# Optimization experiments

Measured on AMD Instinct MI355X. Metric: run time of the kernel, lower is better.

The kernel has to match this reference:

```python
import jax, jax.numpy as jnp
import numpy as np

N_CLASSES = 2  # FS-MOL binary labels


def setup_inputs() -> dict:
    key = jax.random.key(0)
    k1, k2, k3 = jax.random.split(key, 3)
    Ns, Nq, d = 512, 16384, 512
    support_features = jax.random.normal(k1, (Ns, d), dtype=jnp.float32)
    support_labels = jax.random.randint(k2, (Ns,), 0, N_CLASSES, dtype=jnp.int64)
    query_features = jax.random.normal(k3, (Nq, d), dtype=jnp.float32)
    return {
        "support_features": support_features,
        "support_labels": support_labels,
        "query_features": query_features,
    }


def _cov(x):
    # rowvar=False covariance of [N, d] -> [d, d], matching _estimate_cov
    xc = x - jnp.mean(x, axis=0, keepdims=True)
    return (xc.T @ xc) / (x.shape[0] - 1)


def reference(support_features, support_labels, query_features):
    d = support_features.shape[1]
    dt = support_features.dtype
    task_cov = _cov(support_features)          # [d, d]
    reg = jnp.asarray(0.1, dt) * jnp.eye(d, dtype=dt)

    def per_class(c):
        mask = (support_labels == c).astype(dt)            # [Ns]
        n = mask.sum()                                      # scalar count
        mean = (mask[:, None] * support_features).sum(0) / n
        xc = (support_features - mean) * mask[:, None]      # zero out other classes
        cov_c = (xc.T @ xc) / (n - 1.0)
        lam = jnp.minimum(n / (n + 1.0), jnp.asarray(0.1, dt))
        prec = jnp.linalg.inv(lam * cov_c + (1.0 - lam) * task_cov + reg)
        return mean, prec

    means, precs = jax.vmap(per_class)(jnp.arange(N_CLASSES))  # [C,d], [C,d,d]

    # Mahalanobis: diff[c,q,:] = mean_c - query_q  (matches repeated_class_means - repeated_target)
    diff = means[:, None, :] - query_features[None, :, :]      # [C, Nq, d]
    h = jnp.einsum('cqd,cde->cqe', diff, precs)                # [C, Nq, d]
    logits = -(h * diff).sum(-1).T                             # [Nq, C]
    return logits
```

## Files before the change

kernel.cpp:

```cpp
#include <hip/hip_runtime.h>

#define NS 512
#define DF 512
#define NQ 16384

#define WS_MEAN0 0
#define WS_MEAN1 512
#define WS_MEANA 1024
#define WS_CNT   1536
#define WS_V0    2048
#define WS_V1    2560
#define WS_KC    3072
#define WS_M     4096
#define WS_PB    (WS_M + 2*DF*DF)
#define WS_QB    (WS_PB + DF*DF)
#define WS_GP    WS_QB
#define WS_SCR   WS_QB

typedef __attribute__((ext_vector_type(8))) short short8;
typedef __attribute__((ext_vector_type(4))) float floatx4;

__device__ __forceinline__ unsigned short f2bf(float f) {
    unsigned u = __float_as_uint(f);
    unsigned r = (u + 0x7fffu + ((u >> 16) & 1u)) >> 16;
    return (unsigned short)r;
}

__device__ __forceinline__ float readlane_f(float v, int lane) {
    return __uint_as_float(__builtin_amdgcn_readlane(__float_as_uint(v), lane));
}

__device__ __forceinline__ void load_lds16(const void* g, void* l) {
    __builtin_amdgcn_global_load_lds(
        (const __attribute__((address_space(1))) unsigned int*)g,
        (__attribute__((address_space(3))) unsigned int*)l, 16, 0, 0);
}

__device__ __forceinline__ void gj_invert64(float* T, float (*rbuf)[4][64], int tid) {
    int jl = tid & 63, w = tid >> 6;
    float Tr[16];
    if (w < 4) {
#pragma unroll
        for (int m = 0; m < 16; ++m) Tr[m] = T[(w * 16 + m) * 66 + jl];
    }
#pragma unroll
    for (int r = 0; r < 16; ++r) {
        const int q0 = r * 4;
        const int par = r & 1;
        if (w == (q0 >> 4)) {
            const int mb = q0 & 15;
            rbuf[par][0][jl] = Tr[mb + 0];
            rbuf[par][1][jl] = Tr[mb + 1];
            rbuf[par][2][jl] = Tr[mb + 2];
            rbuf[par][3][jl] = Tr[mb + 3];
        }
        __syncthreads();
        if (w < 4) {
            float B[4][4];
#pragma unroll
            for (int a = 0; a < 4; ++a)
#pragma unroll
                for (int bb = 0; bb < 4; ++bb) B[a][bb] = rbuf[par][a][q0 + bb];
#pragma unroll
            for (int p = 0; p < 4; ++p) {
                float piv = 1.0f / B[p][p];
#pragma unroll
                for (int j = 0; j < 4; ++j) if (j != p) B[p][j] *= piv;
#pragma unroll
                for (int i = 0; i < 4; ++i) if (i != p) {
                    float f = B[i][p];
#pragma unroll
                    for (int j = 0; j < 4; ++j) if (j != p) B[i][j] -= f * B[p][j];
                    B[i][p] = -f * piv;
                }
                B[p][p] = piv;
            }
            float r0v = rbuf[par][0][jl], r1v = rbuf[par][1][jl];
            float r2v = rbuf[par][2][jl], r3v = rbuf[par][3][jl];
            float nr[4];
#pragma unroll
            for (int a = 0; a < 4; ++a)
                nr[a] = B[a][0] * r0v + B[a][1] * r1v + B[a][2] * r2v + B[a][3] * r3v;
            bool colin = ((jl >> 2) == r);
            int bsel = jl & 3;
            float Bc[4];
#pragma unroll
            for (int a = 0; a < 4; ++a)
                Bc[a] = bsel == 0 ? B[a][0]
                      : (bsel == 1 ? B[a][1] : (bsel == 2 ? B[a][2] : B[a][3]));
#pragma unroll
            for (int m = 0; m < 16; ++m) {
                float cv0 = readlane_f(Tr[m], q0 + 0);
                float cv1 = readlane_f(Tr[m], q0 + 1);
                float cv2 = readlane_f(Tr[m], q0 + 2);
                float cv3 = readlane_f(Tr[m], q0 + 3);
                float g = Tr[m] - (cv0 * nr[0] + cv1 * nr[1] + cv2 * nr[2] + cv3 * nr[3]);
                bool rowin = (((w * 16 + m) >> 2) == r);
                float gcol = -(cv0 * Bc[0] + cv1 * Bc[1] + cv2 * Bc[2] + cv3 * Bc[3]);
                if (rowin) g = nr[m & 3];
                if (colin) g = rowin ? Bc[m & 3] : gcol;
                Tr[m] = g;
            }
        }
    }
    if (w < 4) {
#pragma unroll
        for (int m = 0; m < 16; ++m) T[(w * 16 + m) * 66 + jl] = Tr[m];
    }
    __syncthreads();
}

__global__ __launch_bounds__(256) void k_front(const float* __restrict__ S,
                                               const int* __restrict__ lab,
                                               float* __restrict__ ws) {
    int b = blockIdx.x, tid = threadIdx.x;
    if (b >= 512) {
        __shared__ int slb[NS];
        __shared__ float r0[4][64], r1[4][64];
        __shared__ int rc[4];
        int bs = b - 512;
        for (int l = tid; l < NS; l += 256) slb[l] = lab[l];
        __syncthreads();
        int dl = tid & 63, ch = tid >> 6;
        int dd = bs * 64 + dl;
        float s0 = 0.f, s1 = 0.f;
        int n1 = 0;
        for (int n = ch * 128; n < ch * 128 + 128; ++n) {
            float v = S[n * DF + dd];
            if (slb[n]) { s1 += v; n1++; } else { s0 += v; }
        }
        r0[ch][dl] = s0; r1[ch][dl] = s1;
        if (dl == 0) rc[ch] = n1;
        __syncthreads();
        if (ch == 0) {
            float t0 = 0.f, t1 = 0.f; int n1t = 0;
#pragma unroll
            for (int x = 0; x < 4; ++x) { t0 += r0[x][dl]; t1 += r1[x][dl]; n1t += rc[x]; }
            float fn1 = (float)n1t, fn0 = (float)(NS - n1t);
            ws[WS_MEAN0 + dd] = t0 / fn0;
            ws[WS_MEAN1 + dd] = t1 / fn1;
            ws[WS_MEANA + dd] = (t0 + t1) / (float)NS;
            if (bs == 0 && dl == 0) {
                ws[WS_CNT] = fn0; ws[WS_CNT + 1] = fn1;
                ws[WS_KC] = 0.f; ws[WS_KC + 1] = 0.f;
            }
        }
        return;
    }
    __shared__ float SA[16 * 65];
    __shared__ float SB[16 * 65];
    __shared__ int lb[16];
    int tx = tid & 15, ty = tid >> 4;
    int i0 = (b & 7) * 64, j0 = ((b >> 3) & 7) * 64;
    int z = b >> 6;
    float a0[4][4] = {{0.f}}, a1[4][4] = {{0.f}};
    for (int nc = z * 64; nc < z * 64 + 64; nc += 16) {
#pragma unroll
        for (int l = 0; l < 4; ++l) {
            int idx = tid + 256 * l;
            int nn = idx >> 6, col = idx & 63;
            SA[nn * 65 + col] = S[(nc + nn) * DF + i0 + col];
            SB[nn * 65 + col] = S[(nc + nn) * DF + j0 + col];
        }
        if (tid < 16) lb[tid] = lab[nc + tid];
        __syncthreads();
#pragma unroll
        for (int kk = 0; kk < 16; ++kk) {
            float av[4], bv[4];
#pragma unroll
            for (int r = 0; r < 4; ++r) av[r] = SA[kk * 65 + ty * 4 + r];
#pragma unroll
            for (int s = 0; s < 4; ++s) bv[s] = SB[kk * 65 + tx * 4 + s];
            if (lb[kk]) {
#pragma unroll
                for (int r = 0; r < 4; ++r)
#pragma unroll
                    for (int s = 0; s < 4; ++s) a1[r][s] += av[r] * bv[s];
            } else {
#pragma unroll
                for (int r = 0; r < 4; ++r)
#pragma unroll
                    for (int s = 0; s < 4; ++s) a0[r][s] += av[r] * bv[s];
            }
        }
        __syncthreads();
    }
    float* Gp = ws + WS_GP;
#pragma unroll
    for (int r = 0; r < 4; ++r) {
        int i = i0 + ty * 4 + r;
#pragma unroll
        for (int s = 0; s < 4; ++s) {
            int j = j0 + tx * 4 + s;
            Gp[((z * 2 + 0) * DF + i) * DF + j] = a0[r][s];
            Gp[((z * 2 + 1) * DF + i) * DF + j] = a1[r][s];
        }
    }
}

__global__ __launch_bounds__(256) void k_asm(float* __restrict__ ws) {
    const float* Gp = ws + WS_GP;
    int e = blockIdx.x * 256 + threadIdx.x;
    int i = e >> 9, j = e & 511;
    float g0 = 0.f, g1 = 0.f;
#pragma unroll
    for (int ch = 0; ch < 8; ++ch) {
        g0 += Gp[((ch * 2 + 0) * DF + i) * DF + j];
        g1 += Gp[((ch * 2 + 1) * DF + i) * DF + j];
    }
    float n0 = ws[WS_CNT], n1 = ws[WS_CNT + 1];
    float lam0 = fminf(n0 / (n0 + 1.f), 0.1f);
    float lam1 = fminf(n1 / (n1 + 1.f), 0.1f);
    float m0i = ws[WS_MEAN0 + i], m1i = ws[WS_MEAN1 + i], mai = ws[WS_MEANA + i];
    float m0j = ws[WS_MEAN0 + j], m1j = ws[WS_MEAN1 + j], maj = ws[WS_MEANA + j];
    float task = (g0 + g1 - (float)NS * mai * maj) / (float)(NS - 1);
    float cov0 = (g0 - n0 * m0i * m0j) / (n0 - 1.f);
    float cov1 = (g1 - n1 * m1i * m1j) / (n1 - 1.f);
    float dg = (i == j) ? 0.1f : 0.f;
    ws[WS_M + i * DF + j] = lam0 * cov0 + (1.f - lam0) * task + dg;
    ws[WS_M + DF * DF + i * DF + j] = lam1 * cov1 + (1.f - lam1) * task + dg;
}

__global__ __launch_bounds__(256) void k_pivot0(float* __restrict__ ws) {
    int c = blockIdx.x;
    __shared__ float T[64 * 66];
    __shared__ float rbuf[2][4][64];
    const float* Akk = ws + WS_M + (size_t)c * DF * DF;
    int tid = threadIdx.x;
#pragma unroll
    for (int m = 0; m < 16; ++m) {
        int idx = tid + 256 * m;
        int i = idx >> 6, j = idx & 63;
        T[i * 66 + j] = Akk[i * DF + j];
    }
    __syncthreads();
    gj_invert64(T, rbuf, tid);
    float* scr = ws + WS_SCR + (0 * 2 + c) * 4096;
#pragma unroll
    for (int m = 0; m < 16; ++m) {
        int idx = tid + 256 * m;
        int i = idx >> 6, j = idx & 63;
        scr[i * 64 + j] = T[i * 66 + j];
    }
}

__global__ __launch_bounds__(512) void k_updA(float* __restrict__ ws, int k, int wbf) {
    int c = blockIdx.y, jh = blockIdx.z;
    int ti = blockIdx.x >> 3, tj = blockIdx.x & 7;
    if (ti == k || tj == k) return;
    float* Mb = ws + WS_M + (size_t)c * DF * DF;
    unsigned short* pb = (unsigned short*)(ws + WS_PB) + (size_t)c * DF * DF;
    const float* scr_in = ws + WS_SCR + ((k & 1) * 2 + c) * 4096;
    int tid = threadIdx.x;
    __shared__ float T[64 * 66];
    __shared__ float LV[64 * 65];
    __shared__ float LU[64 * 34];
    __shared__ float D1[64 * 34];
#pragma unroll
    for (int m = 0; m < 8; ++m) {
        int idx = tid + 512 * m;
        int i = idx >> 6, j = idx & 63;
        T[i * 66 + j] = scr_in[i * 64 + j];
    }
    {
        const float* src = Mb + (ti * 64) * DF + k * 64;
#pragma unroll
        for (int m = 0; m < 8; ++m) {
            int idx = tid + 512 * m;
            int i = idx >> 6, j = idx & 63;
            LV[i * 65 + j] = src[i * DF + j];
        }
    }
    {
        const float* src = Mb + (k * 64) * DF + tj * 64 + jh * 32;
#pragma unroll
        for (int m = 0; m < 4; ++m) {
            int idx = tid + 512 * m;
            int i = idx >> 5, j = idx & 31;
            LU[i * 34 + j] = src[i * DF + j];
        }
    }
    __syncthreads();
    int tx16 = tid & 15, ty32 = tid >> 4;
    int cb0 = jh * 32;
    float a1[2][2] = {{0.f}};
#pragma unroll 8
    for (int kk = 0; kk < 64; ++kk) {
        float av0 = T[(ty32 * 2 + 0) * 66 + kk];
        float av1 = T[(ty32 * 2 + 1) * 66 + kk];
        float2 bv = *(const float2*)&LU[kk * 34 + tx16 * 2];
        a1[0][0] += av0 * bv.x; a1[0][1] += av0 * bv.y;
        a1[1][0] += av1 * bv.x; a1[1][1] += av1 * bv.y;
    }
#pragma unroll
    for (int r = 0; r < 2; ++r)
        *(float2*)&D1[(ty32 * 2 + r) * 34 + tx16 * 2] = make_float2(a1[r][0], a1[r][1]);
    __syncthreads();
    float a2[2][2] = {{0.f}};
#pragma unroll 8
    for (int kk = 0; kk < 64; ++kk) {
        float av0 = LV[(ty32 * 2 + 0) * 65 + kk];
        float av1 = LV[(ty32 * 2 + 1) * 65 + kk];
        float2 bv = *(const float2*)&D1[kk * 34 + tx16 * 2];
        a2[0][0] += av0 * bv.x; a2[0][1] += av0 * bv.y;
        a2[1][0] += av1 * bv.x; a2[1][1] += av1 * bv.y;
    }
    float* dst = Mb + (ti * 64) * DF + tj * 64 + cb0;
#pragma unroll
    for (int r = 0; r < 2; ++r) {
        float2 old = *(const float2*)&dst[(ty32 * 2 + r) * DF + tx16 * 2];
        float nv0 = old.x - a2[r][0], nv1 = old.y - a2[r][1];
        *(float2*)&dst[(ty32 * 2 + r) * DF + tx16 * 2] = make_float2(nv0, nv1);
        if (wbf) {
            unsigned up = (unsigned)f2bf(nv0) | ((unsigned)f2bf(nv1) << 16);
            *(unsigned*)&pb[(size_t)(ti * 64 + ty32 * 2 + r) * DF + tj * 64 + cb0 + tx16 * 2] = up;
        }
    }
}

__global__ __launch_bounds__(512) void k_updB(float* __restrict__ ws, int k, int wbf) {
    int c = blockIdx.y, jh = blockIdx.z;
    int x = blockIdx.x;
    int tid = threadIdx.x;
    __shared__ float T[64 * 66];
    __shared__ float X[64 * 65];
    float* Mb = ws + WS_M + (size_t)c * DF * DF;
    unsigned short* pb = (unsigned short*)(ws + WS_PB) + (size_t)c * DF * DF;
    const float* scr_in = ws + WS_SCR + ((k & 1) * 2 + c) * 4096;

    if (x == 16) {
        if (jh == 1 || k == 7) return;
        const float* src = Mb + ((k + 1) * 64) * DF + (k + 1) * 64;
#pragma unroll
        for (int m = 0; m < 8; ++m) {
            int idx = tid + 512 * m;
            int i = idx >> 6, j = idx & 63;
            T[i * 66 + j] = src[i * DF + j];
        }
        __syncthreads();
        gj_invert64(T, (float(*)[4][64])X, tid);
        float* scr_out = ws + WS_SCR + (((k + 1) & 1) * 2 + c) * 4096;
#pragma unroll
        for (int m = 0; m < 8; ++m) {
            int idx = tid + 512 * m;
            int i = idx >> 6, j = idx & 63;
            scr_out[i * 64 + j] = T[i * 66 + j];
        }
        return;
    }
    int cb0 = jh * 32;
    int tx16 = tid & 15, ty32 = tid >> 4;
    if (x < 8) {
        int tj = x;
        if (tj == k) {
            float* Akk = Mb + (k * 64) * DF + k * 64;
#pragma unroll
            for (int m = 0; m < 4; ++m) {
                int idx = tid + 512 * m;
                int i = idx >> 5, j = idx & 31;
                float v = scr_in[i * 64 + cb0 + j];
                Akk[i * DF + cb0 + j] = v;
                if (wbf) pb[(size_t)(k * 64 + i) * DF + k * 64 + cb0 + j] = f2bf(v);
            }
            return;
        }
#pragma unroll
        for (int m = 0; m < 8; ++m) {
            int idx = tid + 512 * m;
            int i = idx >> 6, j = idx & 63;
            T[i * 66 + j] = scr_in[i * 64 + j];
        }
        {
            const float* src = Mb + (k * 64) * DF + tj * 64 + cb0;
#pragma unroll
            for (int m = 0; m < 4; ++m) {
                int idx = tid + 512 * m;
                int i = idx >> 5, j = idx & 31;
                X[i * 34 + j] = src[i * DF + j];
            }
        }
        __syncthreads();
        float acc[2][2] = {{0.f}};
#pragma unroll 8
        for (int kk = 0; kk < 64; ++kk) {
            float av0 = T[(ty32 * 2 + 0) * 66 + kk];
            float av1 = T[(ty32 * 2 + 1) * 66 + kk];
            float2 bv = *(const float2*)&X[kk * 34 + tx16 * 2];
            acc[0][0] += av0 * bv.x; acc[0][1] += av0 * bv.y;
            acc[1][0] += av1 * bv.x; acc[1][1] += av1 * bv.y;
        }
        float* dst = Mb + (k * 64) * DF + tj * 64 + cb0;
#pragma unroll
        for (int r = 0; r < 2; ++r) {
            *(float2*)&dst[(ty32 * 2 + r) * DF + tx16 * 2] = make_float2(acc[r][0], acc[r][1]);
            if (wbf) {
                unsigned up = (unsigned)f2bf(acc[r][0]) | ((unsigned)f2bf(acc[r][1]) << 16);
                *(unsigned*)&pb[(size_t)(k * 64 + ty32 * 2 + r) * DF + tj * 64 + cb0 + tx16 * 2] = up;
            }
        }
    } else {
        int ti = x - 8;
        if (ti == k || jh == 1) return;
#pragma unroll
        for (int m = 0; m < 8; ++m) {
            int idx = tid + 512 * m;
            int i = idx >> 6, j = idx & 63;
            T[i * 66 + j] = scr_in[i * 64 + j];
        }
        {
            const float* src = Mb + (ti * 64) * DF + k * 64;
#pragma unroll
            for (int m = 0; m < 8; ++m) {
                int idx = tid + 512 * m;
                int i = idx >> 6, j = idx & 63;
                X[i * 65 + j] = src[i * DF + j];
            }
        }
        __syncthreads();
        float acc[2][2][2];
#pragma unroll
        for (int p = 0; p < 2; ++p)
#pragma unroll
            for (int r = 0; r < 2; ++r) { acc[p][r][0] = 0.f; acc[p][r][1] = 0.f; }
#pragma unroll 4
        for (int kk = 0; kk < 64; ++kk) {
            float av0 = X[(ty32 * 2 + 0) * 65 + kk];
            float av1 = X[(ty32 * 2 + 1) * 65 + kk];
            float2 b0 = *(const float2*)&T[kk * 66 + tx16 * 2];
            float2 b1 = *(const float2*)&T[kk * 66 + 32 + tx16 * 2];
            acc[0][0][0] += av0 * b0.x; acc[0][0][1] += av0 * b0.y;
            acc[0][1][0] += av1 * b0.x; acc[0][1][1] += av1 * b0.y;
            acc[1][0][0] += av0 * b1.x; acc[1][0][1] += av0 * b1.y;
            acc[1][1][0] += av1 * b1.x; acc[1][1][1] += av1 * b1.y;
        }
        float* dst = Mb + (ti * 64) * DF + k * 64;
#pragma unroll
        for (int p = 0; p < 2; ++p)
#pragma unroll
            for (int r = 0; r < 2; ++r) {
                int row = ty32 * 2 + r, col = p * 32 + tx16 * 2;
                float v0 = -acc[p][r][0], v1 = -acc[p][r][1];
                *(float2*)&dst[row * DF + col] = make_float2(v0, v1);
                if (wbf) {
                    unsigned up = (unsigned)f2bf(v0) | ((unsigned)f2bf(v1) << 16);
                    *(unsigned*)&pb[(size_t)(ti * 64 + row) * DF + k * 64 + col] = up;
                }
            }
    }
}

__global__ __launch_bounds__(256) void k_vk(float* __restrict__ ws) {
    int c = blockIdx.x >> 3, rb = blockIdx.x & 7;
    const float* P = ws + WS_M + (size_t)c * DF * DF;
    const float* mc = ws + (c ? WS_MEAN1 : WS_MEAN0);
    float* v = ws + (c ? WS_V1 : WS_V0);
    __shared__ float ml[DF];
    __shared__ float red[4][64];
    int tid = threadIdx.x;
    for (int l = tid; l < DF; l += 256) ml[l] = mc[l];
    __syncthreads();
    int rl = tid & 63, ch = tid >> 6;
    int row = rb * 64 + rl;
    float dot = 0.f;
    const float* pr = P + (size_t)row * DF + ch * 128;
    for (int t = 0; t < 32; ++t) {
        float4 pv = *(const float4*)(pr + t * 4);
        const float* mm = ml + ch * 128 + t * 4;
        dot += pv.x * mm[0] + pv.y * mm[1] + pv.z * mm[2] + pv.w * mm[3];
    }
    red[ch][rl] = dot;
    __syncthreads();
    if (ch == 0) {
        float d = red[0][rl] + red[1][rl] + red[2][rl] + red[3][rl];
        v[row] = d;
        float kp = d * ml[row];
#pragma unroll
        for (int off = 32; off > 0; off >>= 1) kp += __shfl_down(kp, off);
        if (rl == 0) atomicAdd(&ws[WS_KC + c], kp);
    }
}

__global__ __launch_bounds__(256) void k_qinit(const float* __restrict__ Q,
                                               float* __restrict__ ws,
                                               float* __restrict__ out) {
    unsigned short* qbw = (unsigned short*)(ws + WS_QB);
    const float* v0 = ws + WS_V0;
    const float* v1 = ws + WS_V1;
    int lane = threadIdx.x & 63;
    int q = blockIdx.x * 4 + (threadIdx.x >> 6);
    const float* qrow = Q + (size_t)q * DF + lane * 8;
    float4 x0 = *(const float4*)(qrow);
    float4 x1 = *(const float4*)(qrow + 4);
    const float* v0p = v0 + lane * 8;
    const float* v1p = v1 + lane * 8;
    float4 w00 = *(const float4*)(v0p), w01 = *(const float4*)(v0p + 4);
    float4 w10 = *(const float4*)(v1p), w11 = *(const float4*)(v1p + 4);
    float a0 = x0.x * w00.x + x0.y * w00.y + x0.z * w00.z + x0.w * w00.w
             + x1.x * w01.x + x1.y * w01.y + x1.z * w01.z + x1.w * w01.w;
    float a1 = x0.x * w10.x + x0.y * w10.y + x0.z * w10.z + x0.w * w10.w
             + x1.x * w11.x + x1.y * w11.y + x1.z * w11.z + x1.w * w11.w;
    short8 r;
    r[0] = (short)f2bf(x0.x); r[1] = (short)f2bf(x0.y);
    r[2] = (short)f2bf(x0.z); r[3] = (short)f2bf(x0.w);
    r[4] = (short)f2bf(x1.x); r[5] = (short)f2bf(x1.y);
    r[6] = (short)f2bf(x1.z); r[7] = (short)f2bf(x1.w);
    *(short8*)(qbw + (size_t)q * DF + lane * 8) = r;
#pragma unroll
    for (int off = 32; off > 0; off >>= 1) {
        a0 += __shfl_down(a0, off);
        a1 += __shfl_down(a1, off);
    }
    if (lane == 0) {
        out[q * 2 + 0] = 2.f * a0 - ws[WS_KC + 0];
        out[q * 2 + 1] = 2.f * a1 - ws[WS_KC + 1];
    }
}

__global__ __launch_bounds__(256, 3) void k_gemm(const float* __restrict__ ws,
                                                 float* __restrict__ out) {
    const unsigned short* qb = (const unsigned short*)(ws + WS_QB);
    int c = blockIdx.y >> 2;
    int n0 = (blockIdx.y & 3) * 128;
    const unsigned short* pbc = (const unsigned short*)(ws + WS_PB) + (size_t)c * DF * DF;
    int q0 = blockIdx.x * 128;
    __shared__ __align__(16) unsigned short Abuf[128 * 64];
    __shared__ __align__(16) unsigned short Bbuf[128 * 64];
    int tid = threadIdx.x;
    int w = tid >> 6, lane = tid & 63;
    int quad = lane >> 4, l15 = lane & 15;
    floatx4 acc[2][8];
#pragma unroll
    for (int mt = 0; mt < 2; ++mt)
#pragma unroll
        for (int nt = 0; nt < 8; ++nt) acc[mt][nt] = (floatx4)(0.f);

    for (int kt = 0; kt < 8; ++kt) {
        int kc2 = kt * 64;
#pragma unroll
        for (int i = 0; i < 4; ++i) {
            int o = tid * 16 + i * 4096;
            int row = o >> 7;
            int sg = ((o >> 4) & 7) ^ (row & 7);
            load_lds16(qb + (size_t)(q0 + row) * DF + kc2 + sg * 8, (char*)Abuf + o);
        }
#pragma unroll
        for (int i = 0; i < 4; ++i) {
            int o = tid * 16 + i * 4096;
            int row = o >> 7;
            int sg = ((o >> 4) & 7) ^ (row & 7);
            load_lds16(pbc + (size_t)(n0 + row) * DF + kc2 + sg * 8, (char*)Bbuf + o);
        }
        __syncthreads();
#pragma unroll
        for (int kk2 = 0; kk2 < 2; ++kk2) {
            int u = ((kk2 * 4 + quad) ^ (l15 & 7)) << 4;
            short8 b[8];
#pragma unroll
            for (int nt = 0; nt < 8; ++nt)
                b[nt] = *(const short8*)((const char*)Bbuf + (nt * 16 + l15) * 128 + u);
#pragma unroll
            for (int mt = 0; mt < 2; ++mt) {
                short8 a = *(const short8*)((const char*)Abuf + (w * 32 + mt * 16 + l15) * 128 + u);
#pragma unroll
                for (int nt = 0; nt < 8; ++nt)
                    acc[mt][nt] = __builtin_amdgcn_mfma_f32_16x16x32_bf16(a, b[nt], acc[mt][nt], 0, 0, 0);
            }
        }
        __syncthreads();
    }
#pragma unroll
    for (int mt = 0; mt < 2; ++mt)
#pragma unroll
        for (int reg = 0; reg < 4; ++reg) {
            int row = w * 32 + mt * 16 + quad * 4 + reg;
            float part = 0.f;
#pragma unroll
            for (int nt = 0; nt < 8; ++nt) {
                float h = acc[mt][nt][reg];
                unsigned qu = qb[(size_t)(q0 + row) * DF + n0 + nt * 16 + l15];
                part += h * __uint_as_float(qu << 16);
            }
            part += __shfl_xor(part, 1);
            part += __shfl_xor(part, 2);
            part += __shfl_xor(part, 4);
            part += __shfl_xor(part, 8);
            if (l15 == 0) atomicAdd(&out[(size_t)(q0 + row) * 2 + c], -part);
        }
}

extern "C" void kernel_launch(void* const* d_in, const int* in_sizes, int n_in,
                              void* d_out, int out_size, void* d_ws, size_t ws_size,
                              hipStream_t stream) {
    const float* S = (const float*)d_in[0];
    const int* lab = (const int*)d_in[1];
    const float* Q = (const float*)d_in[2];
    float* out = (float*)d_out;
    float* ws = (float*)d_ws;

    k_front<<<520, 256, 0, stream>>>(S, lab, ws);
    k_asm<<<1024, 256, 0, stream>>>(ws);
    k_pivot0<<<2, 256, 0, stream>>>(ws);
    for (int k = 0; k < 8; ++k) {
        int wbf = (k == 7) ? 1 : 0;
        k_updA<<<dim3(64, 2, 2), 512, 0, stream>>>(ws, k, wbf);
        k_updB<<<dim3(17, 2, 2), 512, 0, stream>>>(ws, k, wbf);
    }
    k_vk<<<16, 256, 0, stream>>>(ws);
    k_qinit<<<NQ / 4, 256, 0, stream>>>(Q, ws, out);
    k_gemm<<<dim3(NQ / 128, 8), 256, 0, stream>>>(ws, out);
}
```

Measured before the change: 353.3 us.

## Fuse blocked Gauss-Jordan steps into one kernel per pivot with cached panels

Restructures the blocked Gauss-Jordan inversion so that each pivot step runs as a single kernel instead of two. Pivot-row and pivot-column panels are cached in double-buffered workspace, and the next diagonal block is updated and inverted inside the same launch. The first diagonal inversion is folded into a tiled, vectorized assembly kernel, and the bf16 conversion of the precision matrices moves into a separate pass fused with the mean-vector kernel. This removes nine launches and their serialization gaps from the latency-bound inversion chain. In exchange it adds redundant recomputation of the next diagonal block and a more intricate workspace aliasing scheme.

```diff
diff --git a/kernel.cpp b/kernel.cpp
--- a/kernel.cpp
+++ b/kernel.cpp
@@ -15,7 +15,8 @@
 #define WS_PB    (WS_M + 2*DF*DF)
 #define WS_QB    (WS_PB + DF*DF)
 #define WS_GP    WS_QB
-#define WS_SCR   WS_QB
+#define WS_UC    WS_PB
+#define WS_VC    (WS_PB + 2*2*8*4096)
 
 typedef __attribute__((ext_vector_type(8))) short short8;
 typedef __attribute__((ext_vector_type(4))) float floatx4;
@@ -39,10 +40,8 @@
 __device__ __forceinline__ void gj_invert64(float* T, float (*rbuf)[4][64], int tid) {
     int jl = tid & 63, w = tid >> 6;
     float Tr[16];
-    if (w < 4) {
-#pragma unroll
-        for (int m = 0; m < 16; ++m) Tr[m] = T[(w * 16 + m) * 66 + jl];
-    }
+#pragma unroll
+    for (int m = 0; m < 16; ++m) Tr[m] = T[(w * 16 + m) * 66 + jl];
 #pragma unroll
     for (int r = 0; r < 16; ++r) {
         const int q0 = r * 4;
@@ -55,58 +54,54 @@
             rbuf[par][3][jl] = Tr[mb + 3];
         }
         __syncthreads();
-        if (w < 4) {
-            float B[4][4];
-#pragma unroll
-            for (int a = 0; a < 4; ++a)
-#pragma unroll
-                for (int bb = 0; bb < 4; ++bb) B[a][bb] = rbuf[par][a][q0 + bb];
-#pragma unroll
-            for (int p = 0; p < 4; ++p) {
-                float piv = 1.0f / B[p][p];
-#pragma unroll
-                for (int j = 0; j < 4; ++j) if (j != p) B[p][j] *= piv;
-#pragma unroll
-                for (int i = 0; i < 4; ++i) if (i != p) {
-                    float f = B[i][p];
-#pragma unroll
-                    for (int j = 0; j < 4; ++j) if (j != p) B[i][j] -= f * B[p][j];
-                    B[i][p] = -f * piv;
-                }
-                B[p][p] = piv;
-            }
-            float r0v = rbuf[par][0][jl], r1v = rbuf[par][1][jl];
-            float r2v = rbuf[par][2][jl], r3v = rbuf[par][3][jl];
-            float nr[4];
-#pragma unroll
-            for (int a = 0; a < 4; ++a)
-                nr[a] = B[a][0] * r0v + B[a][1] * r1v + B[a][2] * r2v + B[a][3] * r3v;
-            bool colin = ((jl >> 2) == r);
-            int bsel = jl & 3;
-            float Bc[4];
-#pragma unroll
-            for (int a = 0; a < 4; ++a)
-                Bc[a] = bsel == 0 ? B[a][0]
-                      : (bsel == 1 ? B[a][1] : (bsel == 2 ? B[a][2] : B[a][3]));
-#pragma unroll
-            for (int m = 0; m < 16; ++m) {
-                float cv0 = readlane_f(Tr[m], q0 + 0);
-                float cv1 = readlane_f(Tr[m], q0 + 1);
-                float cv2 = readlane_f(Tr[m], q0 + 2);
-                float cv3 = readlane_f(Tr[m], q0 + 3);
-                float g = Tr[m] - (cv0 * nr[0] + cv1 * nr[1] + cv2 * nr[2] + cv3 * nr[3]);
-                bool rowin = (((w * 16 + m) >> 2) == r);
-                float gcol = -(cv0 * Bc[0] + cv1 * Bc[1] + cv2 * Bc[2] + cv3 * Bc[3]);
-                if (rowin) g = nr[m & 3];
-                if (colin) g = rowin ? Bc[m & 3] : gcol;
-                Tr[m] = g;
-            }
-        }
-    }
-    if (w < 4) {
-#pragma unroll
-        for (int m = 0; m < 16; ++m) T[(w * 16 + m) * 66 + jl] = Tr[m];
-    }
+        float B[4][4];
+#pragma unroll
+        for (int a = 0; a < 4; ++a)
+#pragma unroll
+            for (int bb = 0; bb < 4; ++bb) B[a][bb] = rbuf[par][a][q0 + bb];
+#pragma unroll
+        for (int p = 0; p < 4; ++p) {
+            float piv = 1.0f / B[p][p];
+#pragma unroll
+            for (int j = 0; j < 4; ++j) if (j != p) B[p][j] *= piv;
+#pragma unroll
+            for (int i = 0; i < 4; ++i) if (i != p) {
+                float f = B[i][p];
+#pragma unroll
+                for (int j = 0; j < 4; ++j) if (j != p) B[i][j] -= f * B[p][j];
+                B[i][p] = -f * piv;
+            }
+            B[p][p] = piv;
+        }
+        float r0v = rbuf[par][0][jl], r1v = rbuf[par][1][jl];
+        float r2v = rbuf[par][2][jl], r3v = rbuf[par][3][jl];
+        float nr[4];
+#pragma unroll
+        for (int a = 0; a < 4; ++a)
+            nr[a] = B[a][0] * r0v + B[a][1] * r1v + B[a][2] * r2v + B[a][3] * r3v;
+        bool colin = ((jl >> 2) == r);
+        int bsel = jl & 3;
+        float Bc[4];
+#pragma unroll
+        for (int a = 0; a < 4; ++a)
+            Bc[a] = bsel == 0 ? B[a][0]
+                  : (bsel == 1 ? B[a][1] : (bsel == 2 ? B[a][2] : B[a][3]));
+#pragma unroll
+        for (int m = 0; m < 16; ++m) {
+            float cv0 = readlane_f(Tr[m], q0 + 0);
+            float cv1 = readlane_f(Tr[m], q0 + 1);
+            float cv2 = readlane_f(Tr[m], q0 + 2);
+            float cv3 = readlane_f(Tr[m], q0 + 3);
+            float g = Tr[m] - (cv0 * nr[0] + cv1 * nr[1] + cv2 * nr[2] + cv3 * nr[3]);
+            bool rowin = (((w * 16 + m) >> 2) == r);
+            float gcol = -(cv0 * Bc[0] + cv1 * Bc[1] + cv2 * Bc[2] + cv3 * Bc[3]);
+            if (rowin) g = nr[m & 3];
+            if (colin) g = rowin ? Bc[m & 3] : gcol;
+            Tr[m] = g;
+        }
+    }
+#pragma unroll
+    for (int m = 0; m < 16; ++m) T[(w * 16 + m) * 66 + jl] = Tr[m];
     __syncthreads();
 }
 
@@ -199,264 +194,357 @@
 }
 
 __global__ __launch_bounds__(256) void k_asm(float* __restrict__ ws) {
+    int b = blockIdx.x, tid = threadIdx.x;
+    int tx = tid & 15, ty = tid >> 4;
+    __shared__ float T[64 * 66];
+    __shared__ float rbuf[2][4][64];
     const float* Gp = ws + WS_GP;
-    int e = blockIdx.x * 256 + threadIdx.x;
-    int i = e >> 9, j = e & 511;
-    float g0 = 0.f, g1 = 0.f;
-#pragma unroll
-    for (int ch = 0; ch < 8; ++ch) {
-        g0 += Gp[((ch * 2 + 0) * DF + i) * DF + j];
-        g1 += Gp[((ch * 2 + 1) * DF + i) * DF + j];
-    }
     float n0 = ws[WS_CNT], n1 = ws[WS_CNT + 1];
     float lam0 = fminf(n0 / (n0 + 1.f), 0.1f);
     float lam1 = fminf(n1 / (n1 + 1.f), 0.1f);
-    float m0i = ws[WS_MEAN0 + i], m1i = ws[WS_MEAN1 + i], mai = ws[WS_MEANA + i];
-    float m0j = ws[WS_MEAN0 + j], m1j = ws[WS_MEAN1 + j], maj = ws[WS_MEANA + j];
-    float task = (g0 + g1 - (float)NS * mai * maj) / (float)(NS - 1);
-    float cov0 = (g0 - n0 * m0i * m0j) / (n0 - 1.f);
-    float cov1 = (g1 - n1 * m1i * m1j) / (n1 - 1.f);
-    float dg = (i == j) ? 0.1f : 0.f;
-    ws[WS_M + i * DF + j] = lam0 * cov0 + (1.f - lam0) * task + dg;
-    ws[WS_M + DF * DF + i * DF + j] = lam1 * cov1 + (1.f - lam1) * task + dg;
-}
-
-__global__ __launch_bounds__(256) void k_pivot0(float* __restrict__ ws) {
-    int c = blockIdx.x;
-    __shared__ float T[64 * 66];
+    bool dup = (b == 64);
+    int ti = dup ? 0 : (b >> 3), tj = dup ? 0 : (b & 7);
+    int jb = tj * 64 + tx * 4;
+    float4 m0j = *(const float4*)&ws[WS_MEAN0 + jb];
+    float4 m1j = *(const float4*)&ws[WS_MEAN1 + jb];
+    float4 maj = *(const float4*)&ws[WS_MEANA + jb];
+    float out0[4][4], out1[4][4];
+#pragma unroll
+    for (int r = 0; r < 4; ++r) {
+        int i = ti * 64 + ty * 4 + r;
+        float m0i = ws[WS_MEAN0 + i], m1i = ws[WS_MEAN1 + i], mai = ws[WS_MEANA + i];
+        float4 g0 = make_float4(0.f, 0.f, 0.f, 0.f);
+        float4 g1 = make_float4(0.f, 0.f, 0.f, 0.f);
+#pragma unroll
+        for (int ch = 0; ch < 8; ++ch) {
+            float4 a = *(const float4*)&Gp[((ch * 2 + 0) * DF + i) * DF + jb];
+            float4 bb = *(const float4*)&Gp[((ch * 2 + 1) * DF + i) * DF + jb];
+            g0.x += a.x; g0.y += a.y; g0.z += a.z; g0.w += a.w;
+            g1.x += bb.x; g1.y += bb.y; g1.z += bb.z; g1.w += bb.w;
+        }
+        float g0a[4] = {g0.x, g0.y, g0.z, g0.w};
+        float g1a[4] = {g1.x, g1.y, g1.z, g1.w};
+        float m0ja[4] = {m0j.x, m0j.y, m0j.z, m0j.w};
+        float m1ja[4] = {m1j.x, m1j.y, m1j.z, m1j.w};
+        float maja[4] = {maj.x, maj.y, maj.z, maj.w};
+#pragma unroll
+        for (int s = 0; s < 4; ++s) {
+            int j = jb + s;
+            float task = (g0a[s] + g1a[s] - (float)NS * mai * maja[s]) / (float)(NS - 1);
+            float cov0 = (g0a[s] - n0 * m0i * m0ja[s]) / (n0 - 1.f);
+            float cov1 = (g1a[s] - n1 * m1i * m1ja[s]) / (n1 - 1.f);
+            float dg = (i == j) ? 0.1f : 0.f;
+            out0[r][s] = lam0 * cov0 + (1.f - lam0) * task + dg;
+            out1[r][s] = lam1 * cov1 + (1.f - lam1) * task + dg;
+        }
+    }
+    if (!dup) {
+#pragma unroll
+        for (int r = 0; r < 4; ++r) {
+            int i = ti * 64 + ty * 4 + r;
+            *(float4*)&ws[WS_M + (size_t)i * DF + jb] = make_float4(out0[r][0], out0[r][1], out0[r][2], out0[r][3]);
+            *(float4*)&ws[WS_M + DF * DF + (size_t)i * DF + jb] = make_float4(out1[r][0], out1[r][1], out1[r][2], out1[r][3]);
+        }
+        if (ti == 0 && tj != 0) {
+            float* u0 = ws + WS_UC + ((0 * 2 + 0) * 8 + tj) * 4096;
+            float* u1 = ws + WS_UC + ((0 * 2 + 1) * 8 + tj) * 4096;
+#pragma unroll
+            for (int r = 0; r < 4; ++r) {
+                int il = ty * 4 + r, jl = tx * 4;
+                *(float4*)&u0[il * 64 + jl] = make_float4(out0[r][0], out0[r][1], out0[r][2], out0[r][3]);
+                *(float4*)&u1[il * 64 + jl] = make_float4(out1[r][0], out1[r][1], out1[r][2], out1[r][3]);
+            }
+        }
+        if (tj == 0 && ti != 0) {
+            float* v0 = ws + WS_VC + ((0 * 2 + 0) * 8 + ti) * 4096;
+            float* v1 = ws + WS_VC + ((0 * 2 + 1) * 8 + ti) * 4096;
+#pragma unroll
+            for (int r = 0; r < 4; ++r) {
+                int il = ty * 4 + r, jl = tx * 4;
+                *(float4*)&v0[il * 64 + jl] = make_float4(out0[r][0], out0[r][1], out0[r][2], out0[r][3]);
+                *(float4*)&v1[il * 64 + jl] = make_float4(out1[r][0], out1[r][1], out1[r][2], out1[r][3]);
+            }
+        }
+    }
+    if (b == 0 || dup) {
+#pragma unroll
+        for (int r = 0; r < 4; ++r)
+#pragma unroll
+            for (int s = 0; s < 4; ++s)
+                T[(ty * 4 + r) * 66 + tx * 4 + s] = dup ? out1[r][s] : out0[r][s];
+        __syncthreads();
+        gj_invert64(T, rbuf, tid);
+        float* scr = ws + WS_UC + ((0 * 2 + (dup ? 1 : 0)) * 8 + 0) * 4096;
+#pragma unroll
+        for (int m = 0; m < 16; ++m) {
+            int idx = tid + 256 * m;
+            int i = idx >> 6, j = idx & 63;
+            scr[i * 64 + j] = T[i * 66 + j];
+        }
+    }
+}
+
+__global__ __launch_bounds__(256) void k_fgj(float* __restrict__ ws, int k) {
+    int c = blockIdx.y, jh = blockIdx.z;
+    int x = blockIdx.x;
+    int ti = x >> 3, tj = x & 7;
+    int par = k & 1, npar = par ^ 1;
+    int tid = threadIdx.x;
+    int cb0 = jh * 32;
+    float* Mb = ws + WS_M + (size_t)c * DF * DF;
+    const float* UCi = ws + WS_UC + (par * 2 + c) * 8 * 4096;
+    const float* VCi = ws + WS_VC + (par * 2 + c) * 8 * 4096;
+    float* UCo = ws + WS_UC + (npar * 2 + c) * 8 * 4096;
+    float* VCo = ws + WS_VC + (npar * 2 + c) * 8 * 4096;
+    const float* scr_in = UCi + k * 4096;
+
+    if (ti == k && tj == k) {
+        float* Akk = Mb + (k * 64) * DF + k * 64;
+#pragma unroll
+        for (int m = 0; m < 8; ++m) {
+            int idx = tid + 256 * m;
+            int i = idx >> 5, j = idx & 31;
+            Akk[i * DF + cb0 + j] = scr_in[i * 64 + cb0 + j];
+        }
+        return;
+    }
+    bool isrow = (ti == k);
+    bool iscol = (tj == k);
+    bool spec = (ti == k + 1) && (tj == k + 1);
+    if ((iscol || spec) && jh == 1) return;
+
+    __shared__ float T[64 * 68];
+    __shared__ float V[64 * 66];
+    __shared__ float U[64 * 68];
+    __shared__ float D[64 * 68];
     __shared__ float rbuf[2][4][64];
-    const float* Akk = ws + WS_M + (size_t)c * DF * DF;
-    int tid = threadIdx.x;
+
 #pragma unroll
     for (int m = 0; m < 16; ++m) {
         int idx = tid + 256 * m;
         int i = idx >> 6, j = idx & 63;
-        T[i * 66 + j] = Akk[i * DF + j];
-    }
-    __syncthreads();
-    gj_invert64(T, rbuf, tid);
-    float* scr = ws + WS_SCR + (0 * 2 + c) * 4096;
-#pragma unroll
-    for (int m = 0; m < 16; ++m) {
-        int idx = tid + 256 * m;
-        int i = idx >> 6, j = idx & 63;
-        scr[i * 64 + j] = T[i * 66 + j];
-    }
-}
-
-__global__ __launch_bounds__(512) void k_updA(float* __restrict__ ws, int k, int wbf) {
-    int c = blockIdx.y, jh = blockIdx.z;
-    int ti = blockIdx.x >> 3, tj = blockIdx.x & 7;
-    if (ti == k || tj == k) return;
-    float* Mb = ws + WS_M + (size_t)c * DF * DF;
-    unsigned short* pb = (unsigned short*)(ws + WS_PB) + (size_t)c * DF * DF;
-    const float* scr_in = ws + WS_SCR + ((k & 1) * 2 + c) * 4096;
-    int tid = threadIdx.x;
-    __shared__ float T[64 * 66];
-    __shared__ float LV[64 * 65];
-    __shared__ float LU[64 * 34];
-    __shared__ float D1[64 * 34];
-#pragma unroll
-    for (int m = 0; m < 8; ++m) {
-        int idx = tid + 512 * m;
-        int i = idx >> 6, j = idx & 63;
-        T[i * 66 + j] = scr_in[i * 64 + j];
-    }
-    {
-        const float* src = Mb + (ti * 64) * DF + k * 64;
+        T[i * 68 + j] = scr_in[i * 64 + j];
+    }
+
+    if (isrow) {
+        const float* uc = UCi + tj * 4096;
 #pragma unroll
         for (int m = 0; m < 8; ++m) {
-            int idx = tid + 512 * m;
-            int i = idx >> 6, j = idx & 63;
-            LV[i * 65 + j] = src[i * DF + j];
-        }
-    }
-    {
-        const float* src = Mb + (k * 64) * DF + tj * 64 + jh * 32;
-#pragma unroll
-        for (int m = 0; m < 4; ++m) {
-            int idx = tid + 512 * m;
+            int idx = tid + 256 * m;
             int i = idx >> 5, j = idx & 31;
-            LU[i * 34 + j] = src[i * DF + j];
-        }
-    }
-    __syncthreads();
-    int tx16 = tid & 15, ty32 = tid >> 4;
-    int cb0 = jh * 32;
-    float a1[2][2] = {{0.f}};
-#pragma unroll 8
-    for (int kk = 0; kk < 64; ++kk) {
-        float av0 = T[(ty32 * 2 + 0) * 66 + kk];
-        float av1 = T[(ty32 * 2 + 1) * 66 + kk];
-        float2 bv = *(const float2*)&LU[kk * 34 + tx16 * 2];
-        a1[0][0] += av0 * bv.x; a1[0][1] += av0 * bv.y;
-        a1[1][0] += av1 * bv.x; a1[1][1] += av1 * bv.y;
-    }
-#pragma unroll
-    for (int r = 0; r < 2; ++r)
-        *(float2*)&D1[(ty32 * 2 + r) * 34 + tx16 * 2] = make_float2(a1[r][0], a1[r][1]);
-    __syncthreads();
-    float a2[2][2] = {{0.f}};
-#pragma unroll 8
-    for (int kk = 0; kk < 64; ++kk) {
-        float av0 = LV[(ty32 * 2 + 0) * 65 + kk];
-        float av1 = LV[(ty32 * 2 + 1) * 65 + kk];
-        float2 bv = *(const float2*)&D1[kk * 34 + tx16 * 2];
-        a2[0][0] += av0 * bv.x; a2[0][1] += av0 * bv.y;
-        a2[1][0] += av1 * bv.x; a2[1][1] += av1 * bv.y;
-    }
-    float* dst = Mb + (ti * 64) * DF + tj * 64 + cb0;
-#pragma unroll
-    for (int r = 0; r < 2; ++r) {
-        float2 old = *(const float2*)&dst[(ty32 * 2 + r) * DF + tx16 * 2];
-        float nv0 = old.x - a2[r][0], nv1 = old.y - a2[r][1];
-        *(float2*)&dst[(ty32 * 2 + r) * DF + tx16 * 2] = make_float2(nv0, nv1);
-        if (wbf) {
-            unsigned up = (unsigned)f2bf(nv0) | ((unsigned)f2bf(nv1) << 16);
-            *(unsigned*)&pb[(size_t)(ti * 64 + ty32 * 2 + r) * DF + tj * 64 + cb0 + tx16 * 2] = up;
-        }
-    }
-}
-
-__global__ __launch_bounds__(512) void k_updB(float* __restrict__ ws, int k, int wbf) {
-    int c = blockIdx.y, jh = blockIdx.z;
-    int x = blockIdx.x;
-    int tid = threadIdx.x;
-    __shared__ float T[64 * 66];
-    __shared__ float X[64 * 65];
-    float* Mb = ws + WS_M + (size_t)c * DF * DF;
-    unsigned short* pb = (unsigned short*)(ws + WS_PB) + (size_t)c * DF * DF;
-    const float* scr_in = ws + WS_SCR + ((k & 1) * 2 + c) * 4096;
-
-    if (x == 16) {
-        if (jh == 1 || k == 7) return;
-        const float* src = Mb + ((k + 1) * 64) * DF + (k + 1) * 64;
-#pragma unroll
-        for (int m = 0; m < 8; ++m) {
-            int idx = tid + 512 * m;
-            int i = idx >> 6, j = idx & 63;
-            T[i * 66 + j] = src[i * DF + j];
-        }
-        __syncthreads();
-        gj_invert64(T, (float(*)[4][64])X, tid);
-        float* scr_out = ws + WS_SCR + (((k + 1) & 1) * 2 + c) * 4096;
-#pragma unroll
-        for (int m = 0; m < 8; ++m) {
-            int idx = tid + 512 * m;
-            int i = idx >> 6, j = idx & 63;
-            scr_out[i * 64 + j] = T[i * 66 + j];
-        }
-        return;
-    }
-    int cb0 = jh * 32;
-    int tx16 = tid & 15, ty32 = tid >> 4;
-    if (x < 8) {
-        int tj = x;
-        if (tj == k) {
-            float* Akk = Mb + (k * 64) * DF + k * 64;
-#pragma unroll
-            for (int m = 0; m < 4; ++m) {
-                int idx = tid + 512 * m;
-                int i = idx >> 5, j = idx & 31;
-                float v = scr_in[i * 64 + cb0 + j];
-                Akk[i * DF + cb0 + j] = v;
-                if (wbf) pb[(size_t)(k * 64 + i) * DF + k * 64 + cb0 + j] = f2bf(v);
-            }
-            return;
-        }
-#pragma unroll
-        for (int m = 0; m < 8; ++m) {
-            int idx = tid + 512 * m;
-            int i = idx >> 6, j = idx & 63;
-            T[i * 66 + j] = scr_in[i * 64 + j];
-        }
-        {
-            const float* src = Mb + (k * 64) * DF + tj * 64 + cb0;
-#pragma unroll
-            for (int m = 0; m < 4; ++m) {
-                int idx = tid + 512 * m;
-                int i = idx >> 5, j = idx & 31;
-                X[i * 34 + j] = src[i * DF + j];
-            }
-        }
-        __syncthreads();
-        float acc[2][2] = {{0.f}};
+            U[i * 68 + j] = uc[i * 64 + cb0 + j];
+        }
+        __syncthreads();
+        int tx8 = tid & 7, ty32 = tid >> 3;
+        float acc[2][4] = {{0.f}};
 #pragma unroll 8
         for (int kk = 0; kk < 64; ++kk) {
-            float av0 = T[(ty32 * 2 + 0) * 66 + kk];
-            float av1 = T[(ty32 * 2 + 1) * 66 + kk];
-            float2 bv = *(const float2*)&X[kk * 34 + tx16 * 2];
-            acc[0][0] += av0 * bv.x; acc[0][1] += av0 * bv.y;
-            acc[1][0] += av1 * bv.x; acc[1][1] += av1 * bv.y;
+            float a0 = T[(ty32 * 2 + 0) * 68 + kk];
+            float a1 = T[(ty32 * 2 + 1) * 68 + kk];
+            float4 bv = *(const float4*)&U[kk * 68 + tx8 * 4];
+            acc[0][0] += a0 * bv.x; acc[0][1] += a0 * bv.y; acc[0][2] += a0 * bv.z; acc[0][3] += a0 * bv.w;
+            acc[1][0] += a1 * bv.x; acc[1][1] += a1 * bv.y; acc[1][2] += a1 * bv.z; acc[1][3] += a1 * bv.w;
         }
         float* dst = Mb + (k * 64) * DF + tj * 64 + cb0;
 #pragma unroll
         for (int r = 0; r < 2; ++r) {
-            *(float2*)&dst[(ty32 * 2 + r) * DF + tx16 * 2] = make_float2(acc[r][0], acc[r][1]);
-            if (wbf) {
-                unsigned up = (unsigned)f2bf(acc[r][0]) | ((unsigned)f2bf(acc[r][1]) << 16);
-                *(unsigned*)&pb[(size_t)(k * 64 + ty32 * 2 + r) * DF + tj * 64 + cb0 + tx16 * 2] = up;
-            }
-        }
-    } else {
-        int ti = x - 8;
-        if (ti == k || jh == 1) return;
+            int row = ty32 * 2 + r;
+            float4 o = make_float4(acc[r][0], acc[r][1], acc[r][2], acc[r][3]);
+            *(float4*)&dst[row * DF + tx8 * 4] = o;
+            if (tj == k + 1)
+                *(float4*)&VCo[k * 4096 + row * 64 + cb0 + tx8 * 4] = o;
+        }
+        return;
+    }
+
+    if (iscol) {
+        const float* vc = VCi + ti * 4096;
+#pragma unroll
+        for (int m = 0; m < 16; ++m) {
+            int idx = tid + 256 * m;
+            int i = idx >> 6, j = idx & 63;
+            V[i * 66 + j] = vc[i * 64 + j];
+        }
+        __syncthreads();
+        int tx16 = tid & 15, ty16 = tid >> 4;
+        float acc[4][4] = {{0.f}};
+#pragma unroll 8
+        for (int kk = 0; kk < 64; ++kk) {
+            float a[4];
+#pragma unroll
+            for (int r = 0; r < 4; ++r) a[r] = V[(ty16 * 4 + r) * 66 + kk];
+            float4 bv = *(const float4*)&T[kk * 68 + tx16 * 4];
+#pragma unroll
+            for (int r = 0; r < 4; ++r) {
+                acc[r][0] += a[r] * bv.x; acc[r][1] += a[r] * bv.y;
+                acc[r][2] += a[r] * bv.z; acc[r][3] += a[r] * bv.w;
+            }
+        }
+        float* dst = Mb + (ti * 64) * DF + k * 64;
+#pragma unroll
+        for (int r = 0; r < 4; ++r) {
+            int row = ty16 * 4 + r;
+            float4 o = make_float4(-acc[r][0], -acc[r][1], -acc[r][2], -acc[r][3]);
+            *(float4*)&dst[row * DF + tx16 * 4] = o;
+            if (ti == k + 1)
+                *(float4*)&UCo[k * 4096 + row * 64 + tx16 * 4] = o;
+        }
+        return;
+    }
+
+    if (!spec) {
+        const float* vc = VCi + ti * 4096;
+#pragma unroll
+        for (int m = 0; m < 16; ++m) {
+            int idx = tid + 256 * m;
+            int i = idx >> 6, j = idx & 63;
+            V[i * 66 + j] = vc[i * 64 + j];
+        }
+        const float* uc = UCi + tj * 4096;
 #pragma unroll
         for (int m = 0; m < 8; ++m) {
-            int idx = tid + 512 * m;
+            int idx = tid + 256 * m;
+            int i = idx >> 5, j = idx & 31;
+            U[i * 68 + j] = uc[i * 64 + cb0 + j];
+        }
+        __syncthreads();
+        int tx8 = tid & 7, ty32 = tid >> 3;
+        float a1[2][4] = {{0.f}};
+#pragma unroll 8
+        for (int kk = 0; kk < 64; ++kk) {
+            float v0 = T[(ty32 * 2 + 0) * 68 + kk];
+            float v1 = T[(ty32 * 2 + 1) * 68 + kk];
+            float4 bv = *(const float4*)&U[kk * 68 + tx8 * 4];
+            a1[0][0] += v0 * bv.x; a1[0][1] += v0 * bv.y; a1[0][2] += v0 * bv.z; a1[0][3] += v0 * bv.w;
+            a1[1][0] += v1 * bv.x; a1[1][1] += v1 * bv.y; a1[1][2] += v1 * bv.z; a1[1][3] += v1 * bv.w;
+        }
+#pragma unroll
+        for (int r = 0; r < 2; ++r)
+            *(float4*)&D[(ty32 * 2 + r) * 68 + tx8 * 4] = make_float4(a1[r][0], a1[r][1], a1[r][2], a1[r][3]);
+        __syncthreads();
+        float a2[2][4] = {{0.f}};
+#pragma unroll 8
+        for (int kk = 0; kk < 64; ++kk) {
+            float v0 = V[(ty32 * 2 + 0) * 66 + kk];
+            float v1 = V[(ty32 * 2 + 1) * 66 + kk];
+            float4 bv = *(const float4*)&D[kk * 68 + tx8 * 4];
+            a2[0][0] += v0 * bv.x; a2[0][1] += v0 * bv.y; a2[0][2] += v0 * bv.z; a2[0][3] += v0 * bv.w;
+            a2[1][0] += v1 * bv.x; a2[1][1] += v1 * bv.y; a2[1][2] += v1 * bv.z; a2[1][3] += v1 * bv.w;
+        }
+        float* dst = Mb + (ti * 64) * DF + tj * 64 + cb0;
+#pragma unroll
+        for (int r = 0; r < 2; ++r) {
+            int row = ty32 * 2 + r;
+            float4 old = *(const float4*)&dst[row * DF + tx8 * 4];
+            float4 nv = make_float4(old.x - a2[r][0], old.y - a2[r][1], old.z - a2[r][2], old.w - a2[r][3]);
+            *(float4*)&dst[row * DF + tx8 * 4] = nv;
+            if (tj == k + 1)
+                *(float4*)&VCo[ti * 4096 + row * 64 + cb0 + tx8 * 4] = nv;
+            if (ti == k + 1)
+                *(float4*)&UCo[tj * 4096 + row * 64 + cb0 + tx8 * 4] = nv;
+        }
+        return;
+    }
+
+    {
+        const float* vc = VCi + (k + 1) * 4096;
+#pragma unroll
+        for (int m = 0; m < 16; ++m) {
+            int idx = tid + 256 * m;
             int i = idx >> 6, j = idx & 63;
-            T[i * 66 + j] = scr_in[i * 64 + j];
-        }
-        {
-            const float* src = Mb + (ti * 64) * DF + k * 64;
-#pragma unroll
-            for (int m = 0; m < 8; ++m) {
-                int idx = tid + 512 * m;
-                int i = idx >> 6, j = idx & 63;
-                X[i * 65 + j] = src[i * DF + j];
-            }
-        }
-        __syncthreads();
-        float acc[2][2][2];
-#pragma unroll
-        for (int p = 0; p < 2; ++p)
-#pragma unroll
-            for (int r = 0; r < 2; ++r) { acc[p][r][0] = 0.f; acc[p][r][1] = 0.f; }
-#pragma unroll 4
+            V[i * 66 + j] = vc[i * 64 + j];
+        }
+        const float* uc = UCi + (k + 1) * 4096;
+#pragma unroll
+        for (int m = 0; m < 16; ++m) {
+            int idx = tid + 256 * m;
+            int i = idx >> 6, j = idx & 63;
+            U[i * 68 + j] = uc[i * 64 + j];
+        }
+        __syncthreads();
+        int tx16 = tid & 15, ty16 = tid >> 4;
+        float d[4][4] = {{0.f}};
+#pragma unroll 8
         for (int kk = 0; kk < 64; ++kk) {
-            float av0 = X[(ty32 * 2 + 0) * 65 + kk];
-            float av1 = X[(ty32 * 2 + 1) * 65 + kk];
-            float2 b0 = *(const float2*)&T[kk * 66 + tx16 * 2];
-            float2 b1 = *(const float2*)&T[kk * 66 + 32 + tx16 * 2];
-            acc[0][0][0] += av0 * b0.x; acc[0][0][1] += av0 * b0.y;
-            acc[0][1][0] += av1 * b0.x; acc[0][1][1] += av1 * b0.y;
-            acc[1][0][0] += av0 * b1.x; acc[1][0][1] += av0 * b1.y;
-            acc[1][1][0] += av1 * b1.x; acc[1][1][1] += av1 * b1.y;
-        }
-        float* dst = Mb + (ti * 64) * DF + k * 64;
-#pragma unroll
-        for (int p = 0; p < 2; ++p)
-#pragma unroll
-            for (int r = 0; r < 2; ++r) {
-                int row = ty32 * 2 + r, col = p * 32 + tx16 * 2;
-                float v0 = -acc[p][r][0], v1 = -acc[p][r][1];
-                *(float2*)&dst[row * DF + col] = make_float2(v0, v1);
-                if (wbf) {
-                    unsigned up = (unsigned)f2bf(v0) | ((unsigned)f2bf(v1) << 16);
-                    *(unsigned*)&pb[(size_t)(ti * 64 + row) * DF + k * 64 + col] = up;
-                }
-            }
-    }
-}
-
-__global__ __launch_bounds__(256) void k_vk(float* __restrict__ ws) {
-    int c = blockIdx.x >> 3, rb = blockIdx.x & 7;
+            float a[4];
+#pragma unroll
+            for (int r = 0; r < 4; ++r) a[r] = T[(ty16 * 4 + r) * 68 + kk];
+            float4 bv = *(const float4*)&U[kk * 68 + tx16 * 4];
+#pragma unroll
+            for (int r = 0; r < 4; ++r) {
+                d[r][0] += a[r] * bv.x; d[r][1] += a[r] * bv.y;
+                d[r][2] += a[r] * bv.z; d[r][3] += a[r] * bv.w;
+            }
+        }
+#pragma unroll
+        for (int r = 0; r < 4; ++r)
+            *(float4*)&D[(ty16 * 4 + r) * 68 + tx16 * 4] = make_float4(d[r][0], d[r][1], d[r][2], d[r][3]);
+        __syncthreads();
+        float y[4][4] = {{0.f}};
+#pragma unroll 8
+        for (int kk = 0; kk < 64; ++kk) {
+            float a[4];
+#pragma unroll
+            for (int r = 0; r < 4; ++r) a[r] = V[(ty16 * 4 + r) * 66 + kk];
+            float4 bv = *(const float4*)&D[kk * 68 + tx16 * 4];
+#pragma unroll
+            for (int r = 0; r < 4; ++r) {
+                y[r][0] += a[r] * bv.x; y[r][1] += a[r] * bv.y;
+                y[r][2] += a[r] * bv.z; y[r][3] += a[r] * bv.w;
+            }
+        }
+        const float* dst = Mb + (size_t)((k + 1) * 64) * DF + (k + 1) * 64;
+        float4 nv[4];
+#pragma unroll
+        for (int r = 0; r < 4; ++r) {
+            int row = ty16 * 4 + r;
+            float4 old = *(const float4*)&dst[row * DF + tx16 * 4];
+            nv[r] = make_float4(old.x - y[r][0], old.y - y[r][1], old.z - y[r][2], old.w - y[r][3]);
+        }
+        __syncthreads();
+#pragma unroll
+        for (int r = 0; r < 4; ++r) {
+            int row = ty16 * 4 + r;
+            V[row * 66 + tx16 * 4 + 0] = nv[r].x;
+            V[row * 66 + tx16 * 4 + 1] = nv[r].y;
+            V[row * 66 + tx16 * 4 + 2] = nv[r].z;
+            V[row * 66 + tx16 * 4 + 3] = nv[r].w;
+        }
+        __syncthreads();
+        gj_invert64(V, rbuf, tid);
+        float* so = UCo + (k + 1) * 4096;
+#pragma unroll
+        for (int m = 0; m < 16; ++m) {
+            int idx = tid + 256 * m;
+            int i = idx >> 6, j = idx & 63;
+            so[i * 64 + j] = V[i * 66 + j];
+        }
+    }
+}
+
+__global__ __launch_bounds__(256) void k_vkbf(float* __restrict__ ws) {
+    int b = blockIdx.x;
+    int tid = threadIdx.x;
+    if (b >= 16) {
+        int e = (b - 16) * 2048 + tid * 8;
+        const float* M = ws + WS_M;
+        unsigned short* pbw = (unsigned short*)(ws + WS_PB);
+        float4 x0 = *(const float4*)&M[e];
+        float4 x1 = *(const float4*)&M[e + 4];
+        short8 r;
+        r[0] = (short)f2bf(x0.x); r[1] = (short)f2bf(x0.y);
+        r[2] = (short)f2bf(x0.z); r[3] = (short)f2bf(x0.w);
+        r[4] = (short)f2bf(x1.x); r[5] = (short)f2bf(x1.y);
+        r[6] = (short)f2bf(x1.z); r[7] = (short)f2bf(x1.w);
+        *(short8*)(pbw + e) = r;
+        return;
+    }
+    int c = b >> 3, rb = b & 7;
     const float* P = ws + WS_M + (size_t)c * DF * DF;
     const float* mc = ws + (c ? WS_MEAN1 : WS_MEAN0);
     float* v = ws + (c ? WS_V1 : WS_V0);
     __shared__ float ml[DF];
     __shared__ float red[4][64];
-    int tid = threadIdx.x;
     for (int l = tid; l < DF; l += 256) ml[l] = mc[l];
     __syncthreads();
     int rl = tid & 63, ch = tid >> 6;
@@ -598,14 +686,10 @@
     float* ws = (float*)d_ws;
 
     k_front<<<520, 256, 0, stream>>>(S, lab, ws);
-    k_asm<<<1024, 256, 0, stream>>>(ws);
-    k_pivot0<<<2, 256, 0, stream>>>(ws);
-    for (int k = 0; k < 8; ++k) {
-        int wbf = (k == 7) ? 1 : 0;
-        k_updA<<<dim3(64, 2, 2), 512, 0, stream>>>(ws, k, wbf);
-        k_updB<<<dim3(17, 2, 2), 512, 0, stream>>>(ws, k, wbf);
-    }
-    k_vk<<<16, 256, 0, stream>>>(ws);
+    k_asm<<<65, 256, 0, stream>>>(ws);
+    for (int k = 0; k < 8; ++k)
+        k_fgj<<<dim3(64, 2, 2), 256, 0, stream>>>(ws, k);
+    k_vkbf<<<272, 256, 0, stream>>>(ws);
     k_qinit<<<NQ / 4, 256, 0, stream>>>(Q, ws, out);
     k_gemm<<<dim3(NQ / 128, 8), 256, 0, stream>>>(ws, out);
 }
```

After: 342.0 us (median of 2 runs). -3.2%, faster.
